# Performance work log

Hardware: AMD Instinct MI355X
Metric: run time of the kernel (lower is better)

Reference implementation:

```python
import jax, jax.numpy as jnp
import numpy as np

N_ROWS = 100000   # sparse matrix rows (nodes)
N_COLS = 8192     # input feature dim
UNITS = 128
NNZ = 2000000     # ~20 nonzeros per row


def setup_inputs() -> dict:
    key = jax.random.key(0)
    k1, k2, k3, k4, k5 = jax.random.split(key, 5)
    vals = jax.random.normal(k1, (NNZ,), dtype=jnp.float32)
    rows = jax.random.randint(k2, (NNZ,), 0, N_ROWS, dtype=jnp.int32)
    cols = jax.random.randint(k3, (NNZ,), 0, N_COLS, dtype=jnp.int32)
    # GlorotUniform-style scale for W, matching the TF initializer statistics
    limit = jnp.sqrt(6.0 / (N_COLS + UNITS)).astype(jnp.float32)
    W = jax.random.uniform(k4, (N_COLS, UNITS), dtype=jnp.float32, minval=-limit, maxval=limit)
    b = jax.random.uniform(k5, (UNITS,), dtype=jnp.float32, minval=-limit, maxval=limit)
    return {"vals": vals, "rows": rows, "cols": cols, "W": W, "b": b, "num_rows": N_ROWS}


def reference(vals, rows, cols, W, b, num_rows):
    # sparse (COO) [num_rows, F] @ dense W [F, units]:
    # gather the W row for each nonzero, scale by the nonzero value,
    # then scatter-add into the output row -> segment_sum over `rows`.
    gathered = W[cols] * vals[:, None]            # [nnz, units]
    out = jax.ops.segment_sum(gathered, rows, num_segments=num_rows)  # [num_rows, units]
    return out + b                                 # bias add (use_bias=True)
```

## Files before the change

### kernel.cpp

```cpp
#include <hip/hip_runtime.h>
#include <hip/hip_fp16.h>


#define UNITS 128
#define SCAN_BLK 1024
#define CH 4096
#define NBC_SLOTS 512
#define FCAP 6912
#define BCAP 6656
#define SPILL_CAP 8192


__global__ __launch_bounds__(256) void setup_kernel(
        const float* __restrict__ W, __half2* __restrict__ Wh,
        int* __restrict__ ccur, int* __restrict__ spill_cnt,
        int nbc, int wn2 ) {
    int t = blockIdx.x * blockDim.x + threadIdx.x;
    if (t < nbc) ccur[t] = t * BCAP;
    if (t == nbc) *spill_cnt = 0;
    int stride = gridDim.x * blockDim.x;
    const float2* W2 = (const float2*)W;
    for (int i = t; i < wn2; i += stride)
        Wh[i] = __float22half2_rn(W2[i]);
}


__global__ __launch_bounds__(256) void partition_kernel(
        const float* __restrict__ vals, const int* __restrict__ rows,
        const int* __restrict__ cols, int* __restrict__ ccur,
        float2* __restrict__ sortedA, int* __restrict__ spill_cnt,
        float2* __restrict__ spill, int nnz, int nbc) {
    __shared__ float2 staged[CH];
    __shared__ unsigned short bktid[CH];
    __shared__ unsigned short invs[CH];
    __shared__ int hist[NBC_SLOTS];
    __shared__ int pref[NBC_SLOTS];
    __shared__ int gdelta[NBC_SLOTS];

    const int t = threadIdx.x;
    const int chunk0 = blockIdx.x * CH;
    int n = nnz - chunk0;
    if (n > CH) n = CH;

    hist[t] = 0; hist[t + 256] = 0;
    __syncthreads();

    for (int r = t; r < n; r += 256) {
        int i = chunk0 + r;
        int row = rows[i];
        int col = cols[i];
        float v = vals[i];
        int b = row >> 8;
        staged[r] = make_float2(v, __int_as_float(col | ((row & 255) << 13)));
        bktid[r] = (unsigned short)b;
        atomicAdd(&hist[b], 1);
    }
    __syncthreads();

    const int b0 = t, b1 = t + 256;
    pref[b0] = hist[b0]; pref[b1] = hist[b1];
    __syncthreads();
    for (int off = 1; off < NBC_SLOTS; off <<= 1) {
        int a0 = (b0 >= off) ? pref[b0 - off] : 0;
        int a1 = (b1 >= off) ? pref[b1 - off] : 0;
        __syncthreads();
        pref[b0] += a0; pref[b1] += a1;
        __syncthreads();
    }

    int c0 = hist[b0], c1 = hist[b1];
    int ex0 = pref[b0] - c0, ex1 = pref[b1] - c1;
    if (b0 < nbc) {
        int g = (c0 > 0) ? atomicAdd(&ccur[b0], c0) : 0;
        gdelta[b0] = g - ex0;
    }
    if (b1 < nbc) {
        int g = (c1 > 0) ? atomicAdd(&ccur[b1], c1) : 0;
        gdelta[b1] = g - ex1;
    }
    __syncthreads();
    hist[b0] = ex0; hist[b1] = ex1;
    __syncthreads();

    for (int r = t; r < n; r += 256) {
        int pos = atomicAdd(&hist[bktid[r]], 1);
        invs[pos] = (unsigned short)r;
    }
    __syncthreads();

    for (int s = t; s < n; s += 256) {
        int i = invs[s];
        float2 e = staged[i];
        int b = bktid[i];
        int dest = gdelta[b] + s;
        if (dest < (b + 1) * BCAP) {
            sortedA[dest] = e;
        } else {
            int sp = atomicAdd(spill_cnt, 1);
            if (sp < SPILL_CAP) {
                int pk = __float_as_int(e.y);
                int row = (b << 8) | ((pk >> 13) & 255);
                spill[sp] = make_float2(e.x, __int_as_float((pk & 8191) | (row << 13)));
            }
        }
    }
}


__global__ __launch_bounds__(1024) void fused_sort_compute_kernel(
        const float2* __restrict__ A, const int* __restrict__ ccur,
        const __half2* __restrict__ Wh, const float* __restrict__ b,
        float* __restrict__ out, const int* __restrict__ spill_cnt,
        const float2* __restrict__ spill, int NR) {
    __shared__ float2 st[FCAP + 4];
    __shared__ int cnt_s[256];
    __shared__ int rs[257];
    __shared__ int spill_n;
    const int t = threadIdx.x;
    const int lane = t & 63;
    const int w = t >> 6;
    const int bb = blockIdx.x;
    const int r0 = bb << 8;
    const int gstart = bb * BCAP;
    int cnt = ccur[bb] - gstart;
    if (cnt > BCAP) cnt = BCAP;

    const float2 bias = ((const float2*)b)[lane];

    if (t < 256) cnt_s[t] = 0;
    if (t == 0) {
        int sn = *spill_cnt;
        spill_n = (sn > SPILL_CAP) ? SPILL_CAP : sn;
    }
    __syncthreads();

    const int* Ai = (const int*)(A + gstart);
    for (int k = t; k < cnt; k += 1024)
        atomicAdd(&cnt_s[(Ai[2 * k + 1] >> 13) & 255], 1);
    __syncthreads();

    if (t < 256) rs[t] = cnt_s[t];
    __syncthreads();
    for (int off = 1; off < 256; off <<= 1) {
        int v = (t < 256 && t >= off) ? rs[t - off] : 0;
        __syncthreads();
        if (t < 256) rs[t] += v;
        __syncthreads();
    }
    int excl = (t < 256) ? rs[t] - cnt_s[t] : 0;
    __syncthreads();
    if (t < 256) { rs[t] = excl; cnt_s[t] = excl; }
    if (t == 0) rs[256] = cnt;
    __syncthreads();

    for (int k = t; k < cnt; k += 1024) {
        float2 e = A[gstart + k];
        int pk = __float_as_int(e.y);
        int p = atomicAdd(&cnt_s[(pk >> 13) & 255], 1);
        st[p] = make_float2(e.x, __int_as_float(pk & 8191));
    }
    __syncthreads();

    const int sn = spill_n;
    int rbeg = w << 4;
    for (int r = rbeg; r < rbeg + 16; ++r) {
        int grow = r0 + r;
        if (grow >= NR) break;
        int s = rs[r], e = rs[r + 1];
        float ax0 = 0.f, ay0 = 0.f, ax1 = 0.f, ay1 = 0.f;
        for (int k = s; k < e; k += 4) {
            float2 p0 = st[k];
            float2 p1 = st[k + 1];
            float2 p2 = st[k + 2];
            float2 p3 = st[k + 3];
            int c0 = __float_as_int(p0.y) & 8191;
            int c1 = __float_as_int(p1.y) & 8191;
            int c2 = __float_as_int(p2.y) & 8191;
            int c3 = __float_as_int(p3.y) & 8191;
            float v0 = p0.x;
            float v1 = (k + 1 < e) ? p1.x : 0.f;
            float v2 = (k + 2 < e) ? p2.x : 0.f;
            float v3 = (k + 3 < e) ? p3.x : 0.f;
            float2 w0 = __half22float2(Wh[c0 * 64 + lane]);
            float2 w1 = __half22float2(Wh[c1 * 64 + lane]);
            float2 w2 = __half22float2(Wh[c2 * 64 + lane]);
            float2 w3 = __half22float2(Wh[c3 * 64 + lane]);
            ax0 += v0 * w0.x; ay0 += v0 * w0.y;
            ax1 += v1 * w1.x; ay1 += v1 * w1.y;
            ax0 += v2 * w2.x; ay0 += v2 * w2.y;
            ax1 += v3 * w3.x; ay1 += v3 * w3.y;
        }
        for (int s2 = 0; s2 < sn; ++s2) {
            float2 es = spill[s2];
            int pk = __float_as_int(es.y);
            if ((pk >> 13) == grow) {
                float2 wv = __half22float2(Wh[(pk & 8191) * 64 + lane]);
                ax0 += es.x * wv.x; ay0 += es.x * wv.y;
            }
        }
        ((float2*)out)[(size_t)grow * 64 + lane] =
            make_float2(ax0 + ax1 + bias.x, ay0 + ay1 + bias.y);
    }
}


__global__ void hist_kernel(const int* __restrict__ rows, int* __restrict__ counts, int nnz) {
    int i = blockIdx.x * blockDim.x + threadIdx.x;
    if (i < nnz) atomicAdd(&counts[rows[i]], 1);
}

__global__ void scan1_kernel(const int* __restrict__ counts, int* __restrict__ tmp,
                             int* __restrict__ bsums, int NR, int NS) {
    __shared__ int s[SCAN_BLK];
    int t = threadIdx.x;
    int i = blockIdx.x * SCAN_BLK + t;
    int x = (i < NR) ? counts[i] : 0;
    s[t] = x;
    __syncthreads();
    for (int off = 1; off < SCAN_BLK; off <<= 1) {
        int v = (t >= off) ? s[t - off] : 0;
        __syncthreads();
        s[t] += v;
        __syncthreads();
    }
    if (i < NS) tmp[i] = s[t] - x;
    if (t == SCAN_BLK - 1) bsums[blockIdx.x] = s[SCAN_BLK - 1];
}

__global__ void scan2_kernel(int* __restrict__ bsums, int nb) {
    if (threadIdx.x == 0 && blockIdx.x == 0) {
        int run = 0;
        for (int i = 0; i < nb; ++i) { int c = bsums[i]; bsums[i] = run; run += c; }
    }
}

__global__ void scan3_kernel(const int* __restrict__ tmp, const int* __restrict__ bsums,
                             int* __restrict__ row_start, int* __restrict__ cursor,
                             int NR, int NS) {
    int i = blockIdx.x * blockDim.x + threadIdx.x;
    if (i < NS) {
        int v = tmp[i] + bsums[i >> 10];
        row_start[i] = v;
        if (i < NR) cursor[i] = v;
    }
}

__global__ void scatter_sort_kernel(const float* __restrict__ vals, const int* __restrict__ rows,
                                    const int* __restrict__ cols, int* __restrict__ cursor,
                                    float2* __restrict__ sorted, int nnz) {
    int i = blockIdx.x * blockDim.x + threadIdx.x;
    if (i < nnz) {
        int r = rows[i];
        int p = atomicAdd(&cursor[r], 1);
        sorted[p] = make_float2(vals[i], __int_as_float(cols[i]));
    }
}

__global__ void compute_kernel(const float2* __restrict__ sorted, const int* __restrict__ row_start,
                               const float* __restrict__ W, const float* __restrict__ b,
                               float* __restrict__ out, int NR) {
    int lane = threadIdx.x & 63;
    int wv = threadIdx.x >> 6;
    int row = blockIdx.x * 4 + wv;
    if (row >= NR) return;
    int start = row_start[row];
    int end   = row_start[row + 1];
    const float2* W2 = (const float2*)W;
    float accx0 = 0.f, accy0 = 0.f, accx1 = 0.f, accy1 = 0.f;
    for (int base = start; base < end; base += 64) {
        int m = end - base;
        if (m > 64) m = 64;
        float2 p = make_float2(0.f, __int_as_float(0));
        if (lane < m) p = sorted[base + lane];
        int vi = __float_as_int(p.x);
        int ci = __float_as_int(p.y);
        int rounds = (m + 3) & ~3;
        for (int j = 0; j < rounds; j += 4) {
            float v0 = __int_as_float(__builtin_amdgcn_readlane(vi, j));
            int   c0 = __builtin_amdgcn_readlane(ci, j);
            float v1 = __int_as_float(__builtin_amdgcn_readlane(vi, j + 1));
            int   c1 = __builtin_amdgcn_readlane(ci, j + 1);
            float v2 = __int_as_float(__builtin_amdgcn_readlane(vi, j + 2));
            int   c2 = __builtin_amdgcn_readlane(ci, j + 2);
            float v3 = __int_as_float(__builtin_amdgcn_readlane(vi, j + 3));
            int   c3 = __builtin_amdgcn_readlane(ci, j + 3);
            float2 w0 = W2[c0 * 64 + lane];
            float2 w1 = W2[c1 * 64 + lane];
            float2 w2 = W2[c2 * 64 + lane];
            float2 w3 = W2[c3 * 64 + lane];
            accx0 += v0 * w0.x; accy0 += v0 * w0.y;
            accx1 += v1 * w1.x; accy1 += v1 * w1.y;
            accx0 += v2 * w2.x; accy0 += v2 * w2.y;
            accx1 += v3 * w3.x; accy1 += v3 * w3.y;
        }
    }
    float2 bb = ((const float2*)b)[lane];
    ((float2*)out)[(size_t)row * 64 + lane] =
        make_float2(accx0 + accx1 + bb.x, accy0 + accy1 + bb.y);
}


__global__ void init_bias_kernel(float* __restrict__ out, const float* __restrict__ b, int total4) {
    const float4* b4 = (const float4*)b;
    float4* out4 = (float4*)out;
    int stride = gridDim.x * blockDim.x;
    for (int j = blockIdx.x * blockDim.x + threadIdx.x; j < total4; j += stride)
        out4[j] = b4[j & 31];
}

__global__ void scatter_atomic_kernel(const float* __restrict__ vals, const int* __restrict__ rows,
                                      const int* __restrict__ cols, const float* __restrict__ W,
                                      float* __restrict__ out, int nnz) {
    long long idx = (long long)blockIdx.x * blockDim.x + threadIdx.x;
    int i = (int)(idx >> 5);
    int c = (int)(idx & 31);
    if (i >= nnz) return;
    int row = rows[i], col = cols[i];
    float v = vals[i];
    float4 w = ((const float4*)W)[col * 32 + c];
    float* o = out + (size_t)row * UNITS + (c << 2);
    atomicAdd(o + 0, v * w.x);
    atomicAdd(o + 1, v * w.y);
    atomicAdd(o + 2, v * w.z);
    atomicAdd(o + 3, v * w.w);
}

extern "C" void kernel_launch(void* const* d_in, const int* in_sizes, int n_in,
                              void* d_out, int out_size, void* d_ws, size_t ws_size,
                              hipStream_t stream) {
    const float* vals = (const float*)d_in[0];
    const int*   rows = (const int*)d_in[1];
    const int*   cols = (const int*)d_in[2];
    const float* W    = (const float*)d_in[3];
    const float* b    = (const float*)d_in[4];
    float* out = (float*)d_out;

    const int nnz = in_sizes[0];
    const int NW  = in_sizes[3];
    const int NR  = out_size / UNITS;
    const int NS  = NR + 1;
    const int NB  = (NS + SCAN_BLK - 1) / SCAN_BLK;
    const int nbc = (NR + 255) >> 8;

    auto align = [](size_t x) { return (x + 255) & ~(size_t)255; };

    size_t off_ccur    = 0;
    size_t off_scnt    = align(off_ccur + (size_t)nbc * 4);
    size_t off_spill   = align(off_scnt + 4);
    size_t off_wh      = align(off_spill + (size_t)SPILL_CAP * 8);
    size_t off_sortedA = align(off_wh + (size_t)NW * 2);
    size_t needed_full = off_sortedA + (size_t)nbc * BCAP * 8;

    size_t t2_counts   = 0;
    size_t t2_tmp      = align(t2_counts + (size_t)NR * 4);
    size_t t2_bsums    = align(t2_tmp    + (size_t)NS * 4);
    size_t t2_rowstart = align(t2_bsums  + (size_t)NB * 4);
    size_t t2_cursor   = align(t2_rowstart + (size_t)NS * 4);
    size_t t2_sorted   = align(t2_cursor + (size_t)NR * 4);
    size_t needed_r2   = t2_sorted + (size_t)nnz * 8;

    char* ws = (char*)d_ws;

    if (ws_size >= needed_full) {
        int*     ccur      = (int*)(ws + off_ccur);
        int*     spill_cnt = (int*)(ws + off_scnt);
        float2*  spill     = (float2*)(ws + off_spill);
        __half2* Wh        = (__half2*)(ws + off_wh);
        float2*  sortedA   = (float2*)(ws + off_sortedA);

        setup_kernel<<<512, 256, 0, stream>>>(W, Wh, ccur, spill_cnt, nbc, NW / 2);
        {
            int grid = (nnz + CH - 1) / CH;
            partition_kernel<<<grid, 256, 0, stream>>>(vals, rows, cols, ccur, sortedA,
                                                       spill_cnt, spill, nnz, nbc);
        }
        fused_sort_compute_kernel<<<nbc, 1024, 0, stream>>>(sortedA, ccur, Wh, b, out,
                                                            spill_cnt, spill, NR);
    } else if (ws_size >= needed_r2) {
        int*    counts    = (int*)(ws + t2_counts);
        int*    tmp       = (int*)(ws + t2_tmp);
        int*    bsums     = (int*)(ws + t2_bsums);
        int*    row_start = (int*)(ws + t2_rowstart);
        int*    cursor    = (int*)(ws + t2_cursor);
        float2* sorted    = (float2*)(ws + t2_sorted);

        hipMemsetAsync(counts, 0, (size_t)NR * 4, stream);
        {
            int block = 256, grid = (nnz + block - 1) / block;
            hist_kernel<<<grid, block, 0, stream>>>(rows, counts, nnz);
        }
        scan1_kernel<<<NB, SCAN_BLK, 0, stream>>>(counts, tmp, bsums, NR, NS);
        scan2_kernel<<<1, 64, 0, stream>>>(bsums, NB);
        {
            int block = 256, grid = (NS + block - 1) / block;
            scan3_kernel<<<grid, block, 0, stream>>>(tmp, bsums, row_start, cursor, NR, NS);
        }
        {
            int block = 256, grid = (nnz + block - 1) / block;
            scatter_sort_kernel<<<grid, block, 0, stream>>>(vals, rows, cols, cursor, sorted, nnz);
        }
        {
            int grid = (NR + 3) / 4;
            compute_kernel<<<grid, 256, 0, stream>>>(sorted, row_start, W, b, out, NR);
        }
    } else {
        int total4 = out_size / 4;
        int block = 256;
        int grid = (total4 + block - 1) / block;
        init_bias_kernel<<<grid, block, 0, stream>>>(out, b, total4);
        long long total_threads = (long long)nnz * 32;
        long long g2 = (total_threads + block - 1) / block;
        scatter_atomic_kernel<<<(int)g2, block, 0, stream>>>(vals, rows, cols, W, out, nnz);
    }
}
```

Baseline: 170.4 us.

## Shrink row buckets to 98 rows and simplify partition scatter

Row buckets shrink from 256 to 98 rows, which gives about 1021 compute blocks of 512 threads instead of 391 blocks of 1024, for more parallelism and smaller LDS use per block. The partition kernel drops its in-LDS staging, scan and inverse permutation. Each element now claims its global slot directly through a shared-memory atomic on a per-block offset, over 8192-element chunks with the row ids held in registers. This removes LDS traffic and barriers, but the global writes become less ordered and the bucket capacity is tighter, so spill-path use may rise.

```diff
diff --git a/kernel.cpp b/kernel.cpp
--- a/kernel.cpp
+++ b/kernel.cpp
@@ -4,10 +4,10 @@
 
 #define UNITS 128
 #define SCAN_BLK 1024
-#define CH 4096
-#define NBC_SLOTS 512
-#define FCAP 6912
-#define BCAP 6656
+#define BROW 98
+#define NBC_PAD 1040
+#define BCAP 2528
+#define CH2 8192
 #define SPILL_CAP 8192
 
 
@@ -25,150 +25,127 @@
 }
 
 
-__global__ __launch_bounds__(256) void partition_kernel(
+__global__ __launch_bounds__(512, 6) void partition_kernel(
         const float* __restrict__ vals, const int* __restrict__ rows,
         const int* __restrict__ cols, int* __restrict__ ccur,
         float2* __restrict__ sortedA, int* __restrict__ spill_cnt,
         float2* __restrict__ spill, int nnz, int nbc) {
-    __shared__ float2 staged[CH];
-    __shared__ unsigned short bktid[CH];
-    __shared__ unsigned short invs[CH];
-    __shared__ int hist[NBC_SLOTS];
-    __shared__ int pref[NBC_SLOTS];
-    __shared__ int gdelta[NBC_SLOTS];
+    __shared__ int hist[NBC_PAD];
 
     const int t = threadIdx.x;
-    const int chunk0 = blockIdx.x * CH;
-    int n = nnz - chunk0;
-    if (n > CH) n = CH;
-
-    hist[t] = 0; hist[t + 256] = 0;
-    __syncthreads();
-
-    for (int r = t; r < n; r += 256) {
-        int i = chunk0 + r;
-        int row = rows[i];
+    const int chunk0 = blockIdx.x * CH2;
+
+    for (int s = t; s < NBC_PAD; s += 512) hist[s] = 0;
+    __syncthreads();
+
+    int rbuf[16];
+#pragma unroll
+    for (int j = 0; j < 16; ++j) {
+        int i = chunk0 + j * 512 + t;
+        int row = (i < nnz) ? rows[i] : -1;
+        rbuf[j] = row;
+        if (row >= 0) atomicAdd(&hist[row / BROW], 1);
+    }
+    __syncthreads();
+
+    for (int s = t; s < nbc; s += 512) {
+        int c = hist[s];
+        int g = (c > 0) ? atomicAdd(&ccur[s], c) : 0;
+        hist[s] = g;
+    }
+    __syncthreads();
+
+#pragma unroll
+    for (int j = 0; j < 16; ++j) {
+        int row = rbuf[j];
+        if (row < 0) continue;
+        int i = chunk0 + j * 512 + t;
+        int bkt = row / BROW;
+        int rowlo = row - bkt * BROW;
+        int dest = atomicAdd(&hist[bkt], 1);
+        float v = vals[i];
         int col = cols[i];
-        float v = vals[i];
-        int b = row >> 8;
-        staged[r] = make_float2(v, __int_as_float(col | ((row & 255) << 13)));
-        bktid[r] = (unsigned short)b;
-        atomicAdd(&hist[b], 1);
-    }
-    __syncthreads();
-
-    const int b0 = t, b1 = t + 256;
-    pref[b0] = hist[b0]; pref[b1] = hist[b1];
-    __syncthreads();
-    for (int off = 1; off < NBC_SLOTS; off <<= 1) {
-        int a0 = (b0 >= off) ? pref[b0 - off] : 0;
-        int a1 = (b1 >= off) ? pref[b1 - off] : 0;
-        __syncthreads();
-        pref[b0] += a0; pref[b1] += a1;
-        __syncthreads();
-    }
-
-    int c0 = hist[b0], c1 = hist[b1];
-    int ex0 = pref[b0] - c0, ex1 = pref[b1] - c1;
-    if (b0 < nbc) {
-        int g = (c0 > 0) ? atomicAdd(&ccur[b0], c0) : 0;
-        gdelta[b0] = g - ex0;
-    }
-    if (b1 < nbc) {
-        int g = (c1 > 0) ? atomicAdd(&ccur[b1], c1) : 0;
-        gdelta[b1] = g - ex1;
-    }
-    __syncthreads();
-    hist[b0] = ex0; hist[b1] = ex1;
-    __syncthreads();
-
-    for (int r = t; r < n; r += 256) {
-        int pos = atomicAdd(&hist[bktid[r]], 1);
-        invs[pos] = (unsigned short)r;
-    }
-    __syncthreads();
-
-    for (int s = t; s < n; s += 256) {
-        int i = invs[s];
-        float2 e = staged[i];
-        int b = bktid[i];
-        int dest = gdelta[b] + s;
-        if (dest < (b + 1) * BCAP) {
-            sortedA[dest] = e;
+        if (dest < (bkt + 1) * BCAP) {
+            sortedA[dest] = make_float2(v, __int_as_float(col | (rowlo << 13)));
         } else {
             int sp = atomicAdd(spill_cnt, 1);
-            if (sp < SPILL_CAP) {
-                int pk = __float_as_int(e.y);
-                int row = (b << 8) | ((pk >> 13) & 255);
-                spill[sp] = make_float2(e.x, __int_as_float((pk & 8191) | (row << 13)));
-            }
-        }
-    }
-}
-
-
-__global__ __launch_bounds__(1024) void fused_sort_compute_kernel(
+            if (sp < SPILL_CAP)
+                spill[sp] = make_float2(v, __int_as_float(col | (row << 13)));
+        }
+    }
+}
+
+
+__global__ __launch_bounds__(512, 8) void fused_sort_compute_kernel(
         const float2* __restrict__ A, const int* __restrict__ ccur,
         const __half2* __restrict__ Wh, const float* __restrict__ b,
         float* __restrict__ out, const int* __restrict__ spill_cnt,
         const float2* __restrict__ spill, int NR) {
-    __shared__ float2 st[FCAP + 4];
-    __shared__ int cnt_s[256];
-    __shared__ int rs[257];
+    __shared__ float2 st[BCAP + 8];
+    __shared__ int cnt_s[128];
+    __shared__ int rs[132];
     __shared__ int spill_n;
     const int t = threadIdx.x;
     const int lane = t & 63;
     const int w = t >> 6;
     const int bb = blockIdx.x;
-    const int r0 = bb << 8;
+    const int r0 = bb * BROW;
     const int gstart = bb * BCAP;
     int cnt = ccur[bb] - gstart;
     if (cnt > BCAP) cnt = BCAP;
 
     const float2 bias = ((const float2*)b)[lane];
 
-    if (t < 256) cnt_s[t] = 0;
+    if (t < 128) cnt_s[t] = 0;
     if (t == 0) {
         int sn = *spill_cnt;
         spill_n = (sn > SPILL_CAP) ? SPILL_CAP : sn;
     }
     __syncthreads();
 
-    const int* Ai = (const int*)(A + gstart);
-    for (int k = t; k < cnt; k += 1024)
-        atomicAdd(&cnt_s[(Ai[2 * k + 1] >> 13) & 255], 1);
-    __syncthreads();
-
-    if (t < 256) rs[t] = cnt_s[t];
-    __syncthreads();
-    for (int off = 1; off < 256; off <<= 1) {
-        int v = (t < 256 && t >= off) ? rs[t - off] : 0;
+    float2 e[5];
+#pragma unroll
+    for (int j = 0; j < 5; ++j) {
+        int k = j * 512 + t;
+        if (k < cnt) {
+            e[j] = A[gstart + k];
+            atomicAdd(&cnt_s[(__float_as_int(e[j].y) >> 13) & 127], 1);
+        }
+    }
+    __syncthreads();
+
+    if (t < 128) rs[t] = cnt_s[t];
+    __syncthreads();
+    for (int off = 1; off < 128; off <<= 1) {
+        int v = (t < 128 && t >= off) ? rs[t - off] : 0;
         __syncthreads();
-        if (t < 256) rs[t] += v;
+        if (t < 128) rs[t] += v;
         __syncthreads();
     }
-    int excl = (t < 256) ? rs[t] - cnt_s[t] : 0;
-    __syncthreads();
-    if (t < 256) { rs[t] = excl; cnt_s[t] = excl; }
-    if (t == 0) rs[256] = cnt;
-    __syncthreads();
-
-    for (int k = t; k < cnt; k += 1024) {
-        float2 e = A[gstart + k];
-        int pk = __float_as_int(e.y);
-        int p = atomicAdd(&cnt_s[(pk >> 13) & 255], 1);
-        st[p] = make_float2(e.x, __int_as_float(pk & 8191));
+    int excl = (t < 128) ? rs[t] - cnt_s[t] : 0;
+    __syncthreads();
+    if (t < 128) { rs[t] = excl; cnt_s[t] = excl; }
+    if (t == 0) rs[128] = cnt;
+    __syncthreads();
+
+#pragma unroll
+    for (int j = 0; j < 5; ++j) {
+        int k = j * 512 + t;
+        if (k < cnt) {
+            int pk = __float_as_int(e[j].y);
+            int p = atomicAdd(&cnt_s[(pk >> 13) & 127], 1);
+            st[p] = make_float2(e[j].x, __int_as_float(pk & 8191));
+        }
     }
     __syncthreads();
 
     const int sn = spill_n;
-    int rbeg = w << 4;
-    for (int r = rbeg; r < rbeg + 16; ++r) {
+    for (int r = w; r < BROW; r += 8) {
         int grow = r0 + r;
         if (grow >= NR) break;
-        int s = rs[r], e = rs[r + 1];
+        int s = rs[r], ee = rs[r + 1];
         float ax0 = 0.f, ay0 = 0.f, ax1 = 0.f, ay1 = 0.f;
-        for (int k = s; k < e; k += 4) {
+        for (int k = s; k < ee; k += 4) {
             float2 p0 = st[k];
             float2 p1 = st[k + 1];
             float2 p2 = st[k + 2];
@@ -178,9 +155,9 @@
             int c2 = __float_as_int(p2.y) & 8191;
             int c3 = __float_as_int(p3.y) & 8191;
             float v0 = p0.x;
-            float v1 = (k + 1 < e) ? p1.x : 0.f;
-            float v2 = (k + 2 < e) ? p2.x : 0.f;
-            float v3 = (k + 3 < e) ? p3.x : 0.f;
+            float v1 = (k + 1 < ee) ? p1.x : 0.f;
+            float v2 = (k + 2 < ee) ? p2.x : 0.f;
+            float v3 = (k + 3 < ee) ? p3.x : 0.f;
             float2 w0 = __half22float2(Wh[c0 * 64 + lane]);
             float2 w1 = __half22float2(Wh[c1 * 64 + lane]);
             float2 w2 = __half22float2(Wh[c2 * 64 + lane]);
@@ -340,7 +317,7 @@
     const int NR  = out_size / UNITS;
     const int NS  = NR + 1;
     const int NB  = (NS + SCAN_BLK - 1) / SCAN_BLK;
-    const int nbc = (NR + 255) >> 8;
+    const int nbc = (NR + BROW - 1) / BROW;
 
     auto align = [](size_t x) { return (x + 255) & ~(size_t)255; };
 
@@ -361,7 +338,7 @@
 
     char* ws = (char*)d_ws;
 
-    if (ws_size >= needed_full) {
+    if (ws_size >= needed_full && nbc <= NBC_PAD) {
         int*     ccur      = (int*)(ws + off_ccur);
         int*     spill_cnt = (int*)(ws + off_scnt);
         float2*  spill     = (float2*)(ws + off_spill);
@@ -370,12 +347,12 @@
 
         setup_kernel<<<512, 256, 0, stream>>>(W, Wh, ccur, spill_cnt, nbc, NW / 2);
         {
-            int grid = (nnz + CH - 1) / CH;
-            partition_kernel<<<grid, 256, 0, stream>>>(vals, rows, cols, ccur, sortedA,
+            int grid = (nnz + CH2 - 1) / CH2;
+            partition_kernel<<<grid, 512, 0, stream>>>(vals, rows, cols, ccur, sortedA,
                                                        spill_cnt, spill, nnz, nbc);
         }
-        fused_sort_compute_kernel<<<nbc, 1024, 0, stream>>>(sortedA, ccur, Wh, b, out,
-                                                            spill_cnt, spill, NR);
+        fused_sort_compute_kernel<<<nbc, 512, 0, stream>>>(sortedA, ccur, Wh, b, out,
+                                                           spill_cnt, spill, NR);
     } else if (ws_size >= needed_r2) {
         int*    counts    = (int*)(ws + t2_counts);
         int*    tmp       = (int*)(ws + t2_tmp);
```

After: 176.7 us. +3.7%, slower.
